# Kernel optimization log

Measured on AMD Instinct MI355X. Metric: run time of the kernel, lower is better.

The kernel has to match this reference:

```python
import jax, jax.numpy as jnp
import numpy as np

GRID_RES = (8, 8, 4)      # probe grid -> 256 probes
GRID_MIN = 0.0
GRID_MAX = 1.0
RES = 128                  # cubemap face resolution (max_res)
N_QUERY = 524288


def _cube_face_uv(d):
    """Map unit directions [N,3] -> (face id [N], u [N], v [N]) with the standard
    OpenGL/nvdiffrast cubemap convention (boundary_mode='cube')."""
    x, y, z = d[:, 0], d[:, 1], d[:, 2]
    ax, ay, az = jnp.abs(x), jnp.abs(y), jnp.abs(z)
    is_x = (ax >= ay) & (ax >= az)
    is_y = (~is_x) & (ay >= az)
    face = jnp.where(is_x, jnp.where(x >= 0, 0, 1),
           jnp.where(is_y, jnp.where(y >= 0, 2, 3),
                           jnp.where(z >= 0, 4, 5))).astype(jnp.int32)
    ma = jnp.maximum(jnp.where(is_x, ax, jnp.where(is_y, ay, az)), 1e-9)
    sc = jnp.where(is_x, jnp.where(x >= 0, -z, z),
         jnp.where(is_y, x, jnp.where(z >= 0, x, -x)))
    tc = jnp.where(is_x, -y, jnp.where(is_y, jnp.where(y >= 0, z, -z), -y))
    u = 0.5 * (sc / ma + 1.0)
    v = 0.5 * (tc / ma + 1.0)
    return face, u, v


def _trilinear_corners(xyz):
    """Faithful port of MultiEnvLight._compute_trilinear_corners.
    xyz: [N,3] -> (corner probe indices [N,8] int32, normalized weights [N,8])."""
    res_f = jnp.array(GRID_RES, dtype=jnp.float32)
    res_i = jnp.array(GRID_RES, dtype=jnp.int32)
    span = jnp.maximum(GRID_MAX - GRID_MIN, 1e-6)
    coord = (xyz - GRID_MIN) / span * (res_f - 1.0)
    coord = jnp.clip(coord, 0.0, res_f - 1.0)
    i0 = jnp.floor(coord).astype(jnp.int32)
    i1 = jnp.minimum(i0 + 1, res_i - 1)
    t = coord - i0.astype(jnp.float32)
    # 8 corner offsets (ox, oy, oz)
    offs = jnp.array([[ox, oy, oz] for ox in (0, 1) for oy in (0, 1) for oz in (0, 1)],
                     dtype=jnp.int32)                                  # [8,3]
    idx = jnp.where(offs[None] == 1, i1[:, None, :], i0[:, None, :])   # [N,8,3]
    w = jnp.prod(jnp.where(offs[None] == 1, t[:, None, :], 1.0 - t[:, None, :]), axis=-1)  # [N,8]
    stride_x = GRID_RES[1] * GRID_RES[2]
    stride_y = GRID_RES[2]
    flat = idx[..., 0] * stride_x + idx[..., 1] * stride_y + idx[..., 2]  # [N,8]
    w = w / jnp.maximum(jnp.sum(w, axis=1, keepdims=True), 1e-8)
    return flat, w


def setup_inputs() -> dict:
    key = jax.random.key(0)
    k1, k2, k3 = jax.random.split(key, 3)
    xyz = jax.random.uniform(k1, (N_QUERY, 3), dtype=jnp.float32)
    l = jax.random.normal(k2, (N_QUERY, 3), dtype=jnp.float32)
    n_probes = GRID_RES[0] * GRID_RES[1] * GRID_RES[2]
    base = jax.random.normal(k3, (n_probes, 6, RES, RES, 3), dtype=jnp.float32)
    return {"xyz": xyz, "l": l, "base": base}


def reference(xyz, l, base):
    """MultiEnvLight forward, 'pure_env' mode: trilinear k-NN probe selection over
    the grid + bilinear cube-texture sampling of each selected probe's cubemap,
    weighted blend, then sigmoid()*10 (EnvLight output transform)."""
    R = RES
    d = l / jnp.maximum(jnp.linalg.norm(l, axis=-1, keepdims=True), 1e-9)
    face, u, v = _cube_face_uv(d)
    # bilinear texel footprint (clamp-to-edge within the face)
    fx = u * R - 0.5
    fy = v * R - 0.5
    x0f = jnp.floor(fx)
    y0f = jnp.floor(fy)
    tx = fx - x0f
    ty = fy - y0f
    x0 = jnp.clip(x0f.astype(jnp.int32), 0, R - 1)
    x1 = jnp.clip(x0f.astype(jnp.int32) + 1, 0, R - 1)
    y0 = jnp.clip(y0f.astype(jnp.int32), 0, R - 1)
    y1 = jnp.clip(y0f.astype(jnp.int32) + 1, 0, R - 1)

    pidx, pw = _trilinear_corners(xyz)                       # [N,8], [N,8]
    probe_off = pidx * (6 * R * R) + face[:, None] * (R * R)  # [N,8]
    tap = jnp.stack([y0 * R + x0, y0 * R + x1, y1 * R + x0, y1 * R + x1], axis=-1)  # [N,4]
    taps = probe_off[:, :, None] + tap[:, None, :]            # [N,8,4]
    tapw = jnp.stack([(1.0 - ty) * (1.0 - tx), (1.0 - ty) * tx,
                      ty * (1.0 - tx), ty * tx], axis=-1)     # [N,4]

    vals = base.reshape(-1, 3)[taps]                          # [N,8,4,3] gather
    bil = jnp.einsum('nt,nptc->npc', tapw, vals)              # bilinear per probe
    light = jnp.einsum('np,npc->nc', pw, bil)                 # blend 8 corner probes
    return jax.nn.sigmoid(light) * 10.0
```

## Files before the change

kernel.cpp:

```cpp
#include <hip/hip_runtime.h>
#include <math.h>

#define RES 128

__global__ __launch_bounds__(256) void mel_kernel(
    const float* __restrict__ xyz, const float* __restrict__ l,
    const float* __restrict__ base, float* __restrict__ out, int n)
{
    int tid = blockIdx.x * blockDim.x + threadIdx.x;
    int q   = tid >> 2;
    int sub = tid & 3;
    if (q >= n) return;

    float lx = l[3*q+0], ly = l[3*q+1], lz = l[3*q+2];
    float nrm = sqrtf(lx*lx + ly*ly + lz*lz);
    float inv = 1.0f / fmaxf(nrm, 1e-9f);
    float dx = lx*inv, dy = ly*inv, dz = lz*inv;

    float ax = fabsf(dx), ay = fabsf(dy), az = fabsf(dz);
    bool is_x = (ax >= ay) && (ax >= az);
    bool is_y = (!is_x) && (ay >= az);

    int face;
    float ma, sc, tc;
    if (is_x) {
        face = (dx >= 0.0f) ? 0 : 1;
        ma = ax;
        sc = (dx >= 0.0f) ? -dz : dz;
        tc = -dy;
    } else if (is_y) {
        face = (dy >= 0.0f) ? 2 : 3;
        ma = ay;
        sc = dx;
        tc = (dy >= 0.0f) ? dz : -dz;
    } else {
        face = (dz >= 0.0f) ? 4 : 5;
        ma = az;
        sc = (dz >= 0.0f) ? dx : -dx;
        tc = -dy;
    }
    ma = fmaxf(ma, 1e-9f);
    float u = 0.5f * (sc / ma + 1.0f);
    float v = 0.5f * (tc / ma + 1.0f);

    float fx = u * (float)RES - 0.5f;
    float fy = v * (float)RES - 0.5f;
    float x0f = floorf(fx), y0f = floorf(fy);
    float tx = fx - x0f, ty = fy - y0f;
    int x0 = min(max((int)x0f,     0), RES-1);
    int x1 = min(max((int)x0f + 1, 0), RES-1);
    int y0 = min(max((int)y0f,     0), RES-1);
    int y1 = min(max((int)y0f + 1, 0), RES-1);

    float px = xyz[3*q+0], py = xyz[3*q+1], pz = xyz[3*q+2];
    float cx = fminf(fmaxf(px * 7.0f, 0.0f), 7.0f);
    float cy = fminf(fmaxf(py * 7.0f, 0.0f), 7.0f);
    float cz = fminf(fmaxf(pz * 3.0f, 0.0f), 3.0f);
    int ix0 = (int)floorf(cx), iy0 = (int)floorf(cy), iz0 = (int)floorf(cz);
    int ix1 = min(ix0 + 1, 7), iy1 = min(iy0 + 1, 7), iz1 = min(iz0 + 1, 3);
    float tgx = cx - (float)ix0, tgy = cy - (float)iy0, tgz = cz - (float)iz0;

    int   ox  = sub >> 1, oy = sub & 1;
    float wxf = ox ? tgx : (1.0f - tgx);
    float wyf = oy ? tgy : (1.0f - tgy);
    int   gxi = ox ? ix1 : ix0;
    int   gyi = oy ? iy1 : iy0;
    float wxy = wxf * wyf;
    float pw0 = wxy * (1.0f - tgz);
    float pw1 = wxy * tgz;
    int   gb  = gxi*32 + gyi*4;
    int   p0  = gb + iz0;
    int   p1  = gb + iz1;

    int toff[4] = { y0*RES + x0, y0*RES + x1, y1*RES + x0, y1*RES + x1 };
    float bw[4];
    bw[0] = (1.0f - ty) * (1.0f - tx);
    bw[1] = (1.0f - ty) * tx;
    bw[2] = ty * (1.0f - tx);
    bw[3] = ty * tx;

    int face_off = face * (RES * RES);
    const float* bp0 = base + (size_t)(p0 * (6 * RES * RES) + face_off) * 3;
    const float* bp1 = base + (size_t)(p1 * (6 * RES * RES) + face_off) * 3;

    float v0[4][3], v1[4][3];
    #pragma unroll
    for (int t = 0; t < 4; ++t) {
        const float* a = bp0 + toff[t] * 3;
        v0[t][0] = a[0]; v0[t][1] = a[1]; v0[t][2] = a[2];
    }
    #pragma unroll
    for (int t = 0; t < 4; ++t) {
        const float* a = bp1 + toff[t] * 3;
        v1[t][0] = a[0]; v1[t][1] = a[1]; v1[t][2] = a[2];
    }

    __builtin_amdgcn_sched_barrier(0);

    float a0 = 0.0f, a1 = 0.0f, a2 = 0.0f;
    #pragma unroll
    for (int t = 0; t < 4; ++t) {
        float w0 = pw0 * bw[t];
        float w1 = pw1 * bw[t];
        a0 += w0 * v0[t][0] + w1 * v1[t][0];
        a1 += w0 * v0[t][1] + w1 * v1[t][1];
        a2 += w0 * v0[t][2] + w1 * v1[t][2];
    }
    float ws = pw0 + pw1;

    a0 += __shfl_xor(a0, 1); a1 += __shfl_xor(a1, 1);
    a2 += __shfl_xor(a2, 1); ws += __shfl_xor(ws, 1);
    a0 += __shfl_xor(a0, 2); a1 += __shfl_xor(a1, 2);
    a2 += __shfl_xor(a2, 2); ws += __shfl_xor(ws, 2);

    if (sub == 0) {
        float winv = 1.0f / fmaxf(ws, 1e-8f);
        a0 *= winv; a1 *= winv; a2 *= winv;
        out[3*q+0] = 10.0f / (1.0f + __expf(-a0));
        out[3*q+1] = 10.0f / (1.0f + __expf(-a1));
        out[3*q+2] = 10.0f / (1.0f + __expf(-a2));
    }
}

extern "C" void kernel_launch(void* const* d_in, const int* in_sizes, int n_in,
                              void* d_out, int out_size, void* d_ws, size_t ws_size,
                              hipStream_t stream) {
    const float* xyz  = (const float*)d_in[0];
    const float* l    = (const float*)d_in[1];
    const float* base = (const float*)d_in[2];
    float* out = (float*)d_out;
    int n = in_sizes[0] / 3;
    int blocks = (n + 63) / 64;
    mel_kernel<<<blocks, 256, 0, stream>>>(xyz, l, base, out, n);
}
```

Measured before the change: 502.3 us.

## Sort queries by probe cell and cube face before gathering for locality

Adds a counting-sort pre-pass (histogram, scan, scatter) that groups queries by their lower probe-grid cell and cube face. The main kernel then processes queries in that permuted order so neighbouring threads gather from the same cubemap faces and hit in cache more often. It also remaps block indices so each XCD gets a contiguous range of sorted slots. The cost is three extra launches, a memset, global atomics and an indirect load per query, with a fallback to the old path when no workspace is given.

After: 687.3 us. +36.8%, slower.

```diff
diff --git a/kernel.cpp b/kernel.cpp
--- a/kernel.cpp
+++ b/kernel.cpp
@@ -1,16 +1,82 @@
 #include <hip/hip_runtime.h>
 #include <math.h>
 
-#define RES 128
+#define RES   128
+#define NBINS 1536
+
+__device__ __forceinline__ int query_bin(const float* __restrict__ xyz,
+                                         const float* __restrict__ l, int q)
+{
+    float lx = l[3*q+0], ly = l[3*q+1], lz = l[3*q+2];
+    float ax = fabsf(lx), ay = fabsf(ly), az = fabsf(lz);
+    bool is_x = (ax >= ay) && (ax >= az);
+    bool is_y = (!is_x) && (ay >= az);
+    int face = is_x ? (lx >= 0.0f ? 0 : 1)
+                    : (is_y ? (ly >= 0.0f ? 2 : 3)
+                            : (lz >= 0.0f ? 4 : 5));
+    float px = xyz[3*q+0], py = xyz[3*q+1], pz = xyz[3*q+2];
+    int ix0 = (int)floorf(fminf(fmaxf(px * 7.0f, 0.0f), 7.0f));
+    int iy0 = (int)floorf(fminf(fmaxf(py * 7.0f, 0.0f), 7.0f));
+    int iz0 = (int)floorf(fminf(fmaxf(pz * 3.0f, 0.0f), 3.0f));
+    return ((ix0 * 8 + iy0) * 4 + iz0) * 6 + face;
+}
+
+__global__ __launch_bounds__(256) void k_count(
+    const float* __restrict__ xyz, const float* __restrict__ l,
+    int n, unsigned* __restrict__ hist)
+{
+    int q = blockIdx.x * 256 + threadIdx.x;
+    if (q >= n) return;
+    atomicAdd(&hist[query_bin(xyz, l, q)], 1u);
+}
+
+__global__ __launch_bounds__(256) void k_scan(
+    const unsigned* __restrict__ hist, unsigned* __restrict__ cursor)
+{
+    __shared__ unsigned s[256];
+    int t = threadIdx.x;
+    unsigned v[6]; unsigned sum = 0;
+    #pragma unroll
+    for (int k = 0; k < 6; ++k) { v[k] = hist[t*6 + k]; sum += v[k]; }
+    s[t] = sum;
+    __syncthreads();
+    for (int off = 1; off < 256; off <<= 1) {
+        unsigned x = (t >= off) ? s[t - off] : 0u;
+        __syncthreads();
+        s[t] += x;
+        __syncthreads();
+    }
+    unsigned base = s[t] - sum;
+    #pragma unroll
+    for (int k = 0; k < 6; ++k) { cursor[t*6 + k] = base; base += v[k]; }
+}
+
+__global__ __launch_bounds__(256) void k_scatter(
+    const float* __restrict__ xyz, const float* __restrict__ l,
+    int n, unsigned* __restrict__ cursor, unsigned* __restrict__ perm)
+{
+    int q = blockIdx.x * 256 + threadIdx.x;
+    if (q >= n) return;
+    unsigned pos = atomicAdd(&cursor[query_bin(xyz, l, q)], 1u);
+    perm[pos] = q;
+}
 
 __global__ __launch_bounds__(256) void mel_kernel(
     const float* __restrict__ xyz, const float* __restrict__ l,
-    const float* __restrict__ base, float* __restrict__ out, int n)
-{
-    int tid = blockIdx.x * blockDim.x + threadIdx.x;
-    int q   = tid >> 2;
-    int sub = tid & 3;
-    if (q >= n) return;
+    const float* __restrict__ base, float* __restrict__ out,
+    const unsigned* __restrict__ perm, int n)
+{
+    int nb  = gridDim.x;
+    int b   = blockIdx.x;
+    int xcd = b & 7, j = b >> 3;
+    int qq  = nb >> 3, r = nb & 7;
+    int slot = ((xcd < r) ? (xcd * (qq + 1)) : (r * (qq + 1) + (xcd - r) * qq)) + j;
+
+    int g    = threadIdx.x >> 2;
+    int sub  = threadIdx.x & 3;
+    int spos = slot * 64 + g;
+    if (spos >= n) return;
+    int q = perm ? (int)perm[spos] : spos;
 
     float lx = l[3*q+0], ly = l[3*q+1], lz = l[3*q+2];
     float nrm = sqrtf(lx*lx + ly*ly + lz*lz);
@@ -94,7 +160,6 @@
         const float* a = bp1 + toff[t] * 3;
         v1[t][0] = a[0]; v1[t][1] = a[1]; v1[t][2] = a[2];
     }
-
     __builtin_amdgcn_sched_barrier(0);
 
     float a0 = 0.0f, a1 = 0.0f, a2 = 0.0f;
@@ -130,6 +195,21 @@
     const float* base = (const float*)d_in[2];
     float* out = (float*)d_out;
     int n = in_sizes[0] / 3;
-    int blocks = (n + 63) / 64;
-    mel_kernel<<<blocks, 256, 0, stream>>>(xyz, l, base, out, n);
-}
+
+    int qblocks = (n + 63) / 64;
+    int nblocks = (n + 255) / 256;
+
+    size_t need = (size_t)NBINS * 4 * 2 + (size_t)n * 4;
+    if (d_ws != nullptr && ws_size >= need) {
+        unsigned* hist   = (unsigned*)d_ws;
+        unsigned* cursor = hist + NBINS;
+        unsigned* perm   = cursor + NBINS;
+        hipMemsetAsync(hist, 0, NBINS * sizeof(unsigned), stream);
+        k_count  <<<nblocks, 256, 0, stream>>>(xyz, l, n, hist);
+        k_scan   <<<1,       256, 0, stream>>>(hist, cursor);
+        k_scatter<<<nblocks, 256, 0, stream>>>(xyz, l, n, cursor, perm);
+        mel_kernel<<<qblocks, 256, 0, stream>>>(xyz, l, base, out, perm, n);
+    } else {
+        mel_kernel<<<qblocks, 256, 0, stream>>>(xyz, l, base, out, nullptr, n);
+    }
+}
```
